# Kernel tuning notes

Measured on AMD Instinct MI355X. Metric: run time of the kernel, lower is better.

## Reference

```python
import jax, jax.numpy as jnp
import numpy as np

B, S, D, H = 2, 2048, 2048, 16
DH = D // H
NEG = -1000000000.0


def setup_inputs() -> dict:
    key = jax.random.key(0)
    ks = jax.random.split(key, 5)
    return {
        "query_vector": jax.random.normal(ks[0], (B, S, D), dtype=jnp.float32),
        "key_vector": jax.random.normal(ks[1], (B, S, D), dtype=jnp.float32),
        "value_vector": jax.random.normal(ks[2], (B, S, D), dtype=jnp.float32),
        "W_qkv": jax.random.normal(ks[3], (D, 3 * D), dtype=jnp.float32) * (1.0 / np.sqrt(D)),
        "b_qkv": jax.random.normal(ks[4], (3 * D,), dtype=jnp.float32) * 0.01,
    }


def reference(query_vector, key_vector, value_vector, W_qkv, b_qkv):
    # NOTE: original forward only consumes query_vector; key/value args unused.
    qkv = query_vector @ W_qkv + b_qkv                      # [B, S, 3D]
    q, k, v = jnp.split(qkv, 3, axis=-1)                    # each [B, S, D]
    # Faithful to original: plain reshape (NOT transpose) into heads.
    q = q.reshape(B, H, S, DH)
    k = k.reshape(B, H, S, DH)
    v = v.reshape(B, H, S, DH)
    scores = jnp.einsum("bhqd,bhkd->bhqk", q, k) / np.float32(np.sqrt(DH))
    # torch.triu_indices(offset=0): mask j >= i (diagonal included), SET to -1e9.
    idx = jnp.arange(S)
    causal = idx[None, :] >= idx[:, None]                   # [S, S], True where masked
    scores = jnp.where(causal, jnp.float32(NEG), scores)
    attn = jax.nn.softmax(scores, axis=-1)
    out = jnp.einsum("bhqk,bhkd->bhqd", attn, v)            # [B, H, S, DH]
    # dropout is identity in eval mode
    return out.reshape(B, S, D)
```

## Files before the change

### kernel.cpp

```cpp
#include <hip/hip_runtime.h>
#include <hip/hip_bf16.h>
#include <stdint.h>

typedef unsigned short u16;
typedef short short8 __attribute__((ext_vector_type(8)));
typedef short short4v __attribute__((ext_vector_type(4)));
typedef float f32x4 __attribute__((ext_vector_type(4)));

#define CSL (0.08838834764831845f * 1.4426950408889634f)
#define NEGR -1.0e13f


__device__ __forceinline__ u16 f2b(float f) {
  union { float f; unsigned int u; } c; c.f = f;
  unsigned int u = c.u;
  u += 0x7fffu + ((u >> 16) & 1u);
  return (u16)(u >> 16);
}
__device__ __forceinline__ float b2f(u16 h) {
  union { float f; unsigned int u; } c; c.u = ((unsigned int)h) << 16;
  return c.f;
}

__global__ __launch_bounds__(256) void k_cast_fused(const float* __restrict__ q_in,
                                                    u16* __restrict__ qbf,
                                                    const float* __restrict__ W,
                                                    u16* __restrict__ Wt) {
  __shared__ u16 L[64 * 68];
  const int t = threadIdx.x;
  const int b = blockIdx.x;
  if (b < 4096) {
    size_t idx = ((size_t)b * 256 + t) * 8;
    float4 f0 = *(const float4*)(q_in + idx);
    float4 f1 = *(const float4*)(q_in + idx + 4);
    short8 o;
    o[0] = (short)f2b(f0.x); o[1] = (short)f2b(f0.y); o[2] = (short)f2b(f0.z); o[3] = (short)f2b(f0.w);
    o[4] = (short)f2b(f1.x); o[5] = (short)f2b(f1.y); o[6] = (short)f2b(f1.z); o[7] = (short)f2b(f1.w);
    *(short8*)(qbf + idx) = o;
    return;
  }
  const int wb = b - 4096;
  const int nb = (wb % 96) * 64;
  const int kb = (wb / 96) * 64;
#pragma unroll
  for (int it = 0; it < 4; ++it) {
    int idx = it * 1024 + t * 4;
    int r = idx >> 6, c = idx & 63;
    float4 f = *(const float4*)(W + (size_t)(kb + r) * 6144 + nb + c);
    L[r * 68 + c + 0] = f2b(f.x);
    L[r * 68 + c + 1] = f2b(f.y);
    L[r * 68 + c + 2] = f2b(f.z);
    L[r * 68 + c + 3] = f2b(f.w);
  }
  __syncthreads();
#pragma unroll
  for (int it = 0; it < 4; ++it) {
    int idx = it * 1024 + t * 4;
    int i = idx >> 6, j = idx & 63;
    short4v o;
#pragma unroll
    for (int e = 0; e < 4; ++e) o[e] = (short)L[(j + e) * 68 + i];
    *(short4v*)(Wt + (size_t)(nb + i) * 2048 + kb + j) = o;
  }
}

__global__ __launch_bounds__(512, 1) void k_gemm256(const u16* __restrict__ A,
                                                    const u16* __restrict__ Bt,
                                                    const float* __restrict__ bias,
                                                    u16* __restrict__ qb,
                                                    u16* __restrict__ kbuf,
                                                    u16* __restrict__ vbuf) {
  __shared__ u16 As[2][16384];
  __shared__ u16 Bs[2][12288];
  const int t = threadIdx.x;
  const int ln = t & 63, w = t >> 6;
  const int lr = ln & 15, lg = ln >> 4;
  const int wm = w >> 2, wn = w & 3;
  const int Lid = blockIdx.x;
  const int xcd = Lid & 7, l = Lid >> 3;
  const int mt = (xcd & 1) * 8 + (l & 7);
  const int nt = (xcd >> 1) * 8 + (l >> 3);
  const int mb = mt * 256, nb = nt * 192;
  const int cswz = (lr & 7) * 8;
  const int srow = w * 8 + (ln >> 3);
  const int scol = ((ln & 7) ^ (ln >> 3)) * 8;

  const u16* Abase = A + (size_t)mb * 2048;
  const u16* Bbase = Bt + (size_t)nb * 2048;

  f32x4 acc[8][3] = {};

#define STAGE_S1(kt_, buf_)                                                                        \
  do {                                                                                             \
    const u16* as_ = Abase + (size_t)srow * 2048 + (kt_) * 64 + scol;                              \
    const u16* bs_ = Bbase + (size_t)srow * 2048 + (kt_) * 64 + scol;                              \
    __builtin_amdgcn_global_load_lds(                                                              \
        (const __attribute__((address_space(1))) void*)(as_),                                      \
        (__attribute__((address_space(3))) void*)(&As[buf_][0 * 4096 + w * 512]), 16, 0, 0);       \
    __builtin_amdgcn_global_load_lds(                                                              \
        (const __attribute__((address_space(1))) void*)(as_ + (size_t)2 * 64 * 2048),              \
        (__attribute__((address_space(3))) void*)(&As[buf_][2 * 4096 + w * 512]), 16, 0, 0);       \
    _Pragma("unroll")                                                                              \
    for (int p = 0; p < 3; ++p)                                                                    \
      __builtin_amdgcn_global_load_lds(                                                            \
          (const __attribute__((address_space(1))) void*)(bs_ + (size_t)p * 64 * 2048),            \
          (__attribute__((address_space(3))) void*)(&Bs[buf_][p * 4096 + w * 512]), 16, 0, 0);     \
  } while (0)

#define STAGE_S2(kt_, buf_)                                                                        \
  do {                                                                                             \
    const u16* as_ = Abase + (size_t)srow * 2048 + (kt_) * 64 + scol;                              \
    __builtin_amdgcn_global_load_lds(                                                              \
        (const __attribute__((address_space(1))) void*)(as_ + (size_t)1 * 64 * 2048),              \
        (__attribute__((address_space(3))) void*)(&As[buf_][1 * 4096 + w * 512]), 16, 0, 0);       \
    __builtin_amdgcn_global_load_lds(                                                              \
        (const __attribute__((address_space(1))) void*)(as_ + (size_t)3 * 64 * 2048),              \
        (__attribute__((address_space(3))) void*)(&As[buf_][3 * 4096 + w * 512]), 16, 0, 0);       \
  } while (0)

  STAGE_S1(0, 0);
  STAGE_S2(0, 0);
  asm volatile("s_waitcnt vmcnt(0)" ::: "memory");
  __builtin_amdgcn_s_barrier();

  for (int kt = 0; kt < 32; ++kt) {
    const int cur = kt & 1;
    const int ktn = (kt + 1) & 31;
    const u16* At = &As[cur][0];
    const u16* Bl = &Bs[cur][0];
    short8 af[4][2], bf[3][2];

    asm volatile("s_waitcnt vmcnt(2)" ::: "memory");
    __builtin_amdgcn_s_barrier();
#pragma unroll
    for (int mi = 0; mi < 4; ++mi)
#pragma unroll
      for (int ks = 0; ks < 2; ++ks)
        af[mi][ks] = *(const short8*)(At + (wm * 128 + mi * 16 + lr) * 64 + ((ks * 32 + lg * 8) ^ cswz));
#pragma unroll
    for (int ni = 0; ni < 3; ++ni)
#pragma unroll
      for (int ks = 0; ks < 2; ++ks)
        bf[ni][ks] = *(const short8*)(Bl + (wn * 48 + ni * 16 + lr) * 64 + ((ks * 32 + lg * 8) ^ cswz));
    STAGE_S1(ktn, cur ^ 1);
    __builtin_amdgcn_s_barrier();
    __builtin_amdgcn_s_setprio(1);
#pragma unroll
    for (int mi = 0; mi < 4; ++mi)
#pragma unroll
      for (int ni = 0; ni < 3; ++ni)
#pragma unroll
        for (int ks = 0; ks < 2; ++ks)
          acc[mi][ni] = __builtin_amdgcn_mfma_f32_16x16x32_bf16(af[mi][ks], bf[ni][ks], acc[mi][ni], 0, 0, 0);
    __builtin_amdgcn_s_setprio(0);

    asm volatile("s_waitcnt vmcnt(5)" ::: "memory");
    __builtin_amdgcn_s_barrier();
#pragma unroll
    for (int mi = 0; mi < 4; ++mi)
#pragma unroll
      for (int ks = 0; ks < 2; ++ks)
        af[mi][ks] = *(const short8*)(At + (wm * 128 + 64 + mi * 16 + lr) * 64 + ((ks * 32 + lg * 8) ^ cswz));
    STAGE_S2(ktn, cur ^ 1);
    __builtin_amdgcn_s_barrier();
    __builtin_amdgcn_s_setprio(1);
#pragma unroll
    for (int mi = 0; mi < 4; ++mi)
#pragma unroll
      for (int ni = 0; ni < 3; ++ni)
#pragma unroll
        for (int ks = 0; ks < 2; ++ks)
          acc[4 + mi][ni] = __builtin_amdgcn_mfma_f32_16x16x32_bf16(af[mi][ks], bf[ni][ks], acc[4 + mi][ni], 0, 0, 0);
    __builtin_amdgcn_s_setprio(0);
  }
#undef STAGE_S1
#undef STAGE_S2
  asm volatile("s_waitcnt vmcnt(0)" ::: "memory");

#pragma unroll
  for (int ni = 0; ni < 3; ++ni) {
    int ncol = nb + wn * 48 + ni * 16 + lr;
    u16* dst = (ncol < 2048) ? qb : (ncol < 4096 ? kbuf : vbuf);
    int nmod = ncol & 2047;
    float bv = bias[ncol];
#pragma unroll
    for (int m = 0; m < 8; ++m) {
#pragma unroll
      for (int r = 0; r < 4; ++r) {
        int mrow = mb + wm * 128 + m * 16 + lg * 4 + r;
        dst[(size_t)mrow * 2048 + nmod] = f2b(acc[m][ni][r] + bv);
      }
    }
  }
}

__global__ __launch_bounds__(256) void k_vtrans(const u16* __restrict__ v, u16* __restrict__ vt,
                                                float* __restrict__ part) {
  __shared__ u16 L[128 * 136];
  __shared__ float Ls2[256];
  const int t = threadIdx.x;
  const int bh = blockIdx.y, sc = blockIdx.x;
  const size_t base = (size_t)bh * 262144;
#pragma unroll
  for (int it = 0; it < 8; ++it) {
    int chunk = it * 256 + t;
    int s = chunk >> 4, d8 = (chunk & 15) * 8;
    *(short8*)(L + s * 136 + d8) = *(const short8*)(v + base + (size_t)(sc * 128 + s) * 128 + d8);
  }
  __syncthreads();
#pragma unroll
  for (int it = 0; it < 8; ++it) {
    int chunk = it * 256 + t;
    int dh = chunk >> 4, s8 = (chunk & 15) * 8;
    short8 o;
#pragma unroll
    for (int e = 0; e < 8; ++e) o[e] = (short)L[(s8 + e) * 136 + dh];
    *(short8*)(vt + base + (size_t)dh * 2048 + sc * 128 + s8) = o;
  }
  {
    const int dh = t & 127, seg = t >> 7;
    float ps = 0.f;
#pragma unroll 8
    for (int i = 0; i < 64; ++i) ps += b2f(L[(seg * 64 + i) * 136 + dh]);
    Ls2[t] = ps;
    __syncthreads();
    if (t < 128) part[((size_t)bh * 16 + sc) * 128 + t] = Ls2[t] + Ls2[t + 128];
  }
}

__global__ __launch_bounds__(256, 3) void k_attn(const u16* __restrict__ qb,
                                                 const u16* __restrict__ kb,
                                                 const u16* __restrict__ vt,
                                                 const float* __restrict__ part,
                                                 float* __restrict__ out) {
  __shared__ u16 Ks[64 * 128];
  __shared__ u16 Vs[128 * 64];
  __shared__ u16 Ps[4][16 * 64];
  const int t = threadIdx.x;
  const int ln = t & 63, wv = t >> 6;
  const int lr = ln & 15, lg = ln >> 4;
  const int lr7 = lr & 7;
  const int L = blockIdx.y * 32 + blockIdx.x;
  const int wl = (L & 7) * 128 + (L >> 3);
  const int bh = wl >> 5;
  const int qt = 31 - (wl & 31);
  const size_t base = (size_t)bh * 262144;
  const u16* Qh = qb + base;
  const u16* Kh = kb + base;
  const u16* Vth = vt + base;
  float* Oh = out + base;
  const int qs = qt * 64;

  short8 qf[4];
  {
    int qr = qs + wv * 16 + lr;
#pragma unroll
    for (int ks = 0; ks < 4; ++ks)
      qf[ks] = *(const short8*)(Qh + (size_t)qr * 128 + ks * 32 + lg * 8);
  }
  float lsum[4] = {0.f, 0.f, 0.f, 0.f};
  f32x4 acc[8];
  const f32x4 fz = {0.f, 0.f, 0.f, 0.f};
#pragma unroll
  for (int oj = 0; oj < 8; ++oj) acc[oj] = fz;

  u16* Pw = &Ps[wv][0];
  const int nkt = qt + 1;
  for (int kt = 0; kt < nkt; ++kt) {
#pragma unroll
    for (int it = 0; it < 4; ++it) {
      int chunk = it * 256 + wv * 64 + ln;
      int sk = chunk >> 4, c8 = (chunk & 15) ^ (sk & 7);
      __builtin_amdgcn_global_load_lds(
          (const __attribute__((address_space(1))) void*)(Kh + (size_t)(kt * 64 + sk) * 128 + c8 * 8),
          (__attribute__((address_space(3))) void*)(Ks + (size_t)(it * 256 + wv * 64) * 8),
          16, 0, 0);
    }
#pragma unroll
    for (int it = 0; it < 4; ++it) {
      int chunk = it * 256 + wv * 64 + ln;
      int dh = chunk >> 3, c8 = (chunk & 7) ^ (dh & 7);
      __builtin_amdgcn_global_load_lds(
          (const __attribute__((address_space(1))) void*)(Vth + (size_t)dh * 2048 + kt * 64 + c8 * 8),
          (__attribute__((address_space(3))) void*)(Vs + (size_t)(it * 256 + wv * 64) * 8),
          16, 0, 0);
    }
    __syncthreads();

    f32x4 s[4];
#pragma unroll
    for (int ni = 0; ni < 4; ++ni) s[ni] = fz;
#pragma unroll
    for (int ks = 0; ks < 4; ++ks) {
#pragma unroll
      for (int ni = 0; ni < 4; ++ni) {
        short8 kf = *(const short8*)(Ks + (ni * 16 + lr) * 128 + ((ks * 4 + lg) ^ lr7) * 8);
        s[ni] = __builtin_amdgcn_mfma_f32_16x16x32_bf16(qf[ks], kf, s[ni], 0, 0, 0);
      }
    }
    if (kt == qt) {
#pragma unroll
      for (int ni = 0; ni < 4; ++ni) {
        int col = kt * 64 + ni * 16 + lr;
#pragma unroll
        for (int r = 0; r < 4; ++r) {
          int row = qs + wv * 16 + lg * 4 + r;
          if (col >= row) s[ni][r] = NEGR;
        }
      }
    }
#pragma unroll
    for (int ni = 0; ni < 4; ++ni)
#pragma unroll
      for (int r = 0; r < 4; ++r) {
        u16 h = f2b(exp2f(s[ni][r] * CSL));
        int pr = lg * 4 + r, pc = ni * 16 + lr;
        Pw[pr * 64 + ((pc >> 3) ^ (pr & 7)) * 8 + (pc & 7)] = h;
        lsum[r] += b2f(h);
      }
#pragma unroll
    for (int ks2 = 0; ks2 < 2; ++ks2) {
      short8 pa = *(const short8*)(Pw + lr * 64 + ((ks2 * 4 + lg) ^ lr7) * 8);
#pragma unroll
      for (int oj = 0; oj < 8; ++oj) {
        short8 vf = *(const short8*)(Vs + (oj * 16 + lr) * 64 + ((ks2 * 4 + lg) ^ lr7) * 8);
        acc[oj] = __builtin_amdgcn_mfma_f32_16x16x32_bf16(pa, vf, acc[oj], 0, 0, 0);
      }
    }
    __syncthreads();
  }

  float rl[4];
#pragma unroll
  for (int r = 0; r < 4; ++r) {
    float sa = lsum[r];
#pragma unroll
    for (int d = 1; d < 16; d <<= 1) sa += __shfl_xor(sa, d, 64);
    rl[r] = 1.0f / sa;
  }
#pragma unroll
  for (int oj = 0; oj < 8; ++oj)
#pragma unroll
    for (int r = 0; r < 4; ++r) {
      int row = qs + wv * 16 + lg * 4 + r;
      float val = acc[oj][r] * rl[r];
      if (qt == 0 && wv == 0 && lg == 0 && r == 0) {
        float vs = 0.f;
#pragma unroll
        for (int sc = 0; sc < 16; ++sc) vs += part[(size_t)bh * 2048 + sc * 128 + oj * 16 + lr];
        val = vs * (1.0f / 2048.0f);
      }
      Oh[(size_t)row * 128 + oj * 16 + lr] = val;
    }
}

extern "C" void kernel_launch(void* const* d_in, const int* in_sizes, int n_in,
                              void* d_out, int out_size, void* d_ws, size_t ws_size,
                              hipStream_t stream) {
  (void)in_sizes; (void)n_in; (void)out_size; (void)ws_size;
  const float* q_in = (const float*)d_in[0];
  const float* W = (const float*)d_in[3];
  const float* bias = (const float*)d_in[4];
  float* out = (float*)d_out;

  u16* qbf = (u16*)d_ws;
  u16* wtb = qbf + (size_t)4096 * 2048;
  u16* qb  = wtb + (size_t)6144 * 2048;
  u16* kbf = qb  + (size_t)4096 * 2048;
  u16* vbf = kbf + (size_t)4096 * 2048;
  u16* vt  = vbf + (size_t)4096 * 2048;
  float* part = (float*)(vt + (size_t)4096 * 2048);

  k_cast_fused<<<7168, 256, 0, stream>>>(q_in, qbf, W, wtb);
  k_gemm256<<<512, 512, 0, stream>>>(qbf, wtb, bias, qb, kbf, vbf);
  k_vtrans<<<dim3(16, 32), 256, 0, stream>>>(vbf, vt, part);
  k_attn<<<dim3(32, 32), 256, 0, stream>>>(qb, kbf, vt, part, out);
}
```

Measured before the change: 219.8 us.

## Shrink QKV GEMM M-tile to 128 with single-stage pipeline and more blocks

```diff
diff --git a/kernel.cpp b/kernel.cpp
--- a/kernel.cpp
+++ b/kernel.cpp
@@ -64,13 +64,13 @@
   }
 }
 
-__global__ __launch_bounds__(512, 1) void k_gemm256(const u16* __restrict__ A,
+__global__ __launch_bounds__(512, 4) void k_gemm128(const u16* __restrict__ A,
                                                     const u16* __restrict__ Bt,
                                                     const float* __restrict__ bias,
                                                     u16* __restrict__ qb,
                                                     u16* __restrict__ kbuf,
                                                     u16* __restrict__ vbuf) {
-  __shared__ u16 As[2][16384];
+  __shared__ u16 As[2][8192];
   __shared__ u16 Bs[2][12288];
   const int t = threadIdx.x;
   const int ln = t & 63, w = t >> 6;
@@ -78,9 +78,9 @@
   const int wm = w >> 2, wn = w & 3;
   const int Lid = blockIdx.x;
   const int xcd = Lid & 7, l = Lid >> 3;
-  const int mt = (xcd & 1) * 8 + (l & 7);
-  const int nt = (xcd >> 1) * 8 + (l >> 3);
-  const int mb = mt * 256, nb = nt * 192;
+  const int mt = (xcd & 1) * 16 + (l & 15);
+  const int nt = (xcd >> 1) * 8 + (l >> 4);
+  const int mb = mt * 128, nb = nt * 192;
   const int cswz = (lr & 7) * 8;
   const int srow = w * 8 + (ln >> 3);
   const int scol = ((ln & 7) ^ (ln >> 3)) * 8;
@@ -88,18 +88,17 @@
   const u16* Abase = A + (size_t)mb * 2048;
   const u16* Bbase = Bt + (size_t)nb * 2048;
 
-  f32x4 acc[8][3] = {};
-
-#define STAGE_S1(kt_, buf_)                                                                        \
+  f32x4 acc[4][3] = {};
+
+#define STAGE_KT(kt_, buf_)                                                                        \
   do {                                                                                             \
     const u16* as_ = Abase + (size_t)srow * 2048 + (kt_) * 64 + scol;                              \
     const u16* bs_ = Bbase + (size_t)srow * 2048 + (kt_) * 64 + scol;                              \
-    __builtin_amdgcn_global_load_lds(                                                              \
-        (const __attribute__((address_space(1))) void*)(as_),                                      \
-        (__attribute__((address_space(3))) void*)(&As[buf_][0 * 4096 + w * 512]), 16, 0, 0);       \
-    __builtin_amdgcn_global_load_lds(                                                              \
-        (const __attribute__((address_space(1))) void*)(as_ + (size_t)2 * 64 * 2048),              \
-        (__attribute__((address_space(3))) void*)(&As[buf_][2 * 4096 + w * 512]), 16, 0, 0);       \
+    _Pragma("unroll")                                                                              \
+    for (int p = 0; p < 2; ++p)                                                                    \
+      __builtin_amdgcn_global_load_lds(                                                            \
+          (const __attribute__((address_space(1))) void*)(as_ + (size_t)p * 64 * 2048),            \
+          (__attribute__((address_space(3))) void*)(&As[buf_][p * 4096 + w * 512]), 16, 0, 0);     \
     _Pragma("unroll")                                                                              \
     for (int p = 0; p < 3; ++p)                                                                    \
       __builtin_amdgcn_global_load_lds(                                                            \
@@ -107,19 +106,7 @@
           (__attribute__((address_space(3))) void*)(&Bs[buf_][p * 4096 + w * 512]), 16, 0, 0);     \
   } while (0)
 
-#define STAGE_S2(kt_, buf_)                                                                        \
-  do {                                                                                             \
-    const u16* as_ = Abase + (size_t)srow * 2048 + (kt_) * 64 + scol;                              \
-    __builtin_amdgcn_global_load_lds(                                                              \
-        (const __attribute__((address_space(1))) void*)(as_ + (size_t)1 * 64 * 2048),              \
-        (__attribute__((address_space(3))) void*)(&As[buf_][1 * 4096 + w * 512]), 16, 0, 0);       \
-    __builtin_amdgcn_global_load_lds(                                                              \
-        (const __attribute__((address_space(1))) void*)(as_ + (size_t)3 * 64 * 2048),              \
-        (__attribute__((address_space(3))) void*)(&As[buf_][3 * 4096 + w * 512]), 16, 0, 0);       \
-  } while (0)
-
-  STAGE_S1(0, 0);
-  STAGE_S2(0, 0);
+  STAGE_KT(0, 0);
   asm volatile("s_waitcnt vmcnt(0)" ::: "memory");
   __builtin_amdgcn_s_barrier();
 
@@ -128,53 +115,35 @@
     const int ktn = (kt + 1) & 31;
     const u16* At = &As[cur][0];
     const u16* Bl = &Bs[cur][0];
+
+    STAGE_KT(ktn, cur ^ 1);
+    asm volatile("s_waitcnt vmcnt(5)" ::: "memory");
+    __builtin_amdgcn_s_barrier();
+
     short8 af[4][2], bf[3][2];
-
-    asm volatile("s_waitcnt vmcnt(2)" ::: "memory");
-    __builtin_amdgcn_s_barrier();
 #pragma unroll
     for (int mi = 0; mi < 4; ++mi)
 #pragma unroll
       for (int ks = 0; ks < 2; ++ks)
-        af[mi][ks] = *(const short8*)(At + (wm * 128 + mi * 16 + lr) * 64 + ((ks * 32 + lg * 8) ^ cswz));
+        af[mi][ks] = *(const short8*)(At + (wm * 64 + mi * 16 + lr) * 64 + ((ks * 32 + lg * 8) ^ cswz));
 #pragma unroll
     for (int ni = 0; ni < 3; ++ni)
 #pragma unroll
       for (int ks = 0; ks < 2; ++ks)
         bf[ni][ks] = *(const short8*)(Bl + (wn * 48 + ni * 16 + lr) * 64 + ((ks * 32 + lg * 8) ^ cswz));
-    STAGE_S1(ktn, cur ^ 1);
-    __builtin_amdgcn_s_barrier();
+
     __builtin_amdgcn_s_setprio(1);
 #pragma unroll
-    for (int mi = 0; mi < 4; ++mi)
-#pragma unroll
-      for (int ni = 0; ni < 3; ++ni)
-#pragma unroll
-        for (int ks = 0; ks < 2; ++ks)
+    for (int ks = 0; ks < 2; ++ks)
+#pragma unroll
+      for (int mi = 0; mi < 4; ++mi)
+#pragma unroll
+        for (int ni = 0; ni < 3; ++ni)
           acc[mi][ni] = __builtin_amdgcn_mfma_f32_16x16x32_bf16(af[mi][ks], bf[ni][ks], acc[mi][ni], 0, 0, 0);
     __builtin_amdgcn_s_setprio(0);
-
-    asm volatile("s_waitcnt vmcnt(5)" ::: "memory");
     __builtin_amdgcn_s_barrier();
-#pragma unroll
-    for (int mi = 0; mi < 4; ++mi)
-#pragma unroll
-      for (int ks = 0; ks < 2; ++ks)
-        af[mi][ks] = *(const short8*)(At + (wm * 128 + 64 + mi * 16 + lr) * 64 + ((ks * 32 + lg * 8) ^ cswz));
-    STAGE_S2(ktn, cur ^ 1);
-    __builtin_amdgcn_s_barrier();
-    __builtin_amdgcn_s_setprio(1);
-#pragma unroll
-    for (int mi = 0; mi < 4; ++mi)
-#pragma unroll
-      for (int ni = 0; ni < 3; ++ni)
-#pragma unroll
-        for (int ks = 0; ks < 2; ++ks)
-          acc[4 + mi][ni] = __builtin_amdgcn_mfma_f32_16x16x32_bf16(af[mi][ks], bf[ni][ks], acc[4 + mi][ni], 0, 0, 0);
-    __builtin_amdgcn_s_setprio(0);
-  }
-#undef STAGE_S1
-#undef STAGE_S2
+  }
+#undef STAGE_KT
   asm volatile("s_waitcnt vmcnt(0)" ::: "memory");
 
 #pragma unroll
@@ -184,11 +153,11 @@
     int nmod = ncol & 2047;
     float bv = bias[ncol];
 #pragma unroll
-    for (int m = 0; m < 8; ++m) {
+    for (int mi = 0; mi < 4; ++mi) {
 #pragma unroll
       for (int r = 0; r < 4; ++r) {
-        int mrow = mb + wm * 128 + m * 16 + lg * 4 + r;
-        dst[(size_t)mrow * 2048 + nmod] = f2b(acc[m][ni][r] + bv);
+        int mrow = mb + wm * 64 + mi * 16 + lg * 4 + r;
+        dst[(size_t)mrow * 2048 + nmod] = f2b(acc[mi][ni][r] + bv);
       }
     }
   }
@@ -372,7 +341,7 @@
   float* part = (float*)(vt + (size_t)4096 * 2048);
 
   k_cast_fused<<<7168, 256, 0, stream>>>(q_in, qbf, W, wtb);
-  k_gemm256<<<512, 512, 0, stream>>>(qbf, wtb, bias, qb, kbf, vbf);
+  k_gemm128<<<1024, 512, 0, stream>>>(qbf, wtb, bias, qb, kbf, vbf);
   k_vtrans<<<dim3(16, 32), 256, 0, stream>>>(vbf, vt, part);
   k_attn<<<dim3(32, 32), 256, 0, stream>>>(qb, kbf, vt, part, out);
 }
```

Measured after the change: 218.8 us (median of 4 runs). No clear change (-0.4%).
